# Performance work log

Hardware: AMD Instinct MI355X
Metric: run time of the kernel (lower is better)

Reference implementation:

```python
import jax, jax.numpy as jnp
import numpy as np

NUM_EMBEDDINGS = 1024
EMBEDDING_DIM = 512
SAMPLE_TOKENS = 4
CODE_DIM = EMBEDDING_DIM // SAMPLE_TOKENS  # 128
COMMITMENT_COST = 0.25


def setup_inputs() -> dict:
    key = jax.random.key(0)
    k1, k2 = jax.random.split(key)
    inputs = jax.random.normal(k1, (16, 1024, EMBEDDING_DIM), dtype=jnp.float32)
    # nn.Embedding weight init: uniform(-1/K, 1/K)
    emb_weight = jax.random.uniform(
        k2, (NUM_EMBEDDINGS, CODE_DIM), dtype=jnp.float32,
        minval=-1.0 / NUM_EMBEDDINGS, maxval=1.0 / NUM_EMBEDDINGS)
    return {"inputs": inputs, "emb_weight": emb_weight}


def reference(inputs, emb_weight):
    input_shape = inputs.shape
    flat = inputs.reshape(-1, CODE_DIM)  # [N, d]
    distances = (jnp.sum(flat * flat, axis=1, keepdims=True)
                 + jnp.sum(emb_weight * emb_weight, axis=1)
                 - 2.0 * jnp.matmul(flat, emb_weight.T))  # [N, K]
    encoding_indices = jnp.argmin(distances, axis=1)  # [N]
    # gather codebook rows instead of one-hot matmul (same math)
    quantized = jnp.take(emb_weight, encoding_indices, axis=0).reshape(input_shape)

    e_latent_loss = jnp.mean((jax.lax.stop_gradient(quantized) - inputs) ** 2)
    q_latent_loss = jnp.mean((quantized - jax.lax.stop_gradient(inputs)) ** 2)
    loss = q_latent_loss + COMMITMENT_COST * e_latent_loss

    # straight-through estimator
    quantized_ste = inputs + jax.lax.stop_gradient(quantized - inputs)

    # avg_probs = mean of one-hot encodings = code-usage histogram / N
    n = flat.shape[0]
    counts = jnp.zeros((NUM_EMBEDDINGS,), dtype=jnp.float32).at[encoding_indices].add(1.0)
    avg_probs = counts / n
    perplexity = jnp.exp(-jnp.sum(avg_probs * jnp.log(avg_probs + 1e-10)))

    return (quantized_ste, loss, perplexity)
```

## Files before the change

### kernel.cpp

```cpp
#include <hip/hip_runtime.h>
#include <cmath>

#define DIM      128
#define NELEMS   8388608
#define BAND_INT 12288

typedef __attribute__((ext_vector_type(8))) short  short8;
typedef __attribute__((ext_vector_type(4))) float  f32x4;


__device__ inline unsigned short f2bf(float x) {
    unsigned u = __float_as_uint(x);
    unsigned r = u + 0x7FFFu + ((u >> 16) & 1u);
    return (unsigned short)(r >> 16);
}

__global__ __launch_bounds__(256) void vq_prep_kernel(
        const float* __restrict__ e, unsigned short* __restrict__ Ehi,
        float* __restrict__ Bsq, int* __restrict__ counts, double* __restrict__ sse) {
    const int tid = threadIdx.x;
    {
        const int t  = blockIdx.x * 256 + tid;
        const int c  = t >> 4;
        const int gs = t & 15;
        const int kt = gs >> 2, qd = gs & 3;
        const int d0 = gs * 8;
        const float4 v0 = *(const float4*)(e + c * DIM + d0);
        const float4 v1 = *(const float4*)(e + c * DIM + d0 + 4);
        float f[8] = {v0.x, v0.y, v0.z, v0.w, v1.x, v1.y, v1.z, v1.w};
        unsigned short h[8];
        #pragma unroll
        for (int j = 0; j < 8; ++j) h[j] = f2bf(f[j]);
        const int ct = c >> 4, n = c & 15;
        uint4 ph;
        ph.x = h[0] | (h[1] << 16); ph.y = h[2] | (h[3] << 16);
        ph.z = h[4] | (h[5] << 16); ph.w = h[6] | (h[7] << 16);
        *(uint4*)&Ehi[(((ct * 4 + kt) * 64 + qd * 16 + n) * 8)] = ph;
    }
    {
        const int lane = tid & 31;
        #pragma unroll
        for (int r2 = 0; r2 < 2; ++r2) {
            const int row = blockIdx.x * 16 + (tid >> 5) * 2 + r2;
            const float4 xv = *(const float4*)(e + (size_t)row * DIM + lane * 4);
            float s = xv.x * xv.x + xv.y * xv.y + xv.z * xv.z + xv.w * xv.w;
            #pragma unroll
            for (int off = 16; off > 0; off >>= 1) s += __shfl_xor(s, off);
            if (lane == 0) Bsq[row] = s;
        }
    }
    if (blockIdx.x == 0) {
        ((int4*)counts)[tid] = make_int4(0, 0, 0, 0);
        if (tid == 0) *sse = 0.0;
    }
}

#define LOADPAIR(BUF, P)                                                        \
    do {                                                                        \
        const unsigned short* _bp = Ehi + (size_t)(P) * 4096;                   \
        _Pragma("unroll")                                                       \
        for (int _c = 0; _c < 2; ++_c)                                          \
            _Pragma("unroll")                                                   \
            for (int _kt = 0; _kt < 4; ++_kt)                                   \
                BUF[_c][_kt] = *(const short8*)&_bp[((_c * 4 + _kt) * 64 + lane) * 8]; \
    } while (0)

#define COMPUTEPAIR(BUF, P)                                                     \
    do {                                                                        \
        _Pragma("unroll")                                                       \
        for (int _c = 0; _c < 2; ++_c) {                                        \
            const int _ct = 2 * (P) + _c;                                       \
            f32x4 _a0 = cinit, _a1 = cinit;                                     \
            _Pragma("unroll")                                                   \
            for (int _kt = 0; _kt < 4; ++_kt) {                                 \
                _a0 = __builtin_amdgcn_mfma_f32_16x16x32_bf16(Af[0][_kt], BUF[_c][_kt], _a0, 0, 0, 0); \
                _a1 = __builtin_amdgcn_mfma_f32_16x16x32_bf16(Af[1][_kt], BUF[_c][_kt], _a1, 0, 0, 0); \
            }                                                                   \
            _Pragma("unroll")                                                   \
            for (int _r = 0; _r < 4; ++_r) {                                    \
                const int _k0 = (__float_as_int(_a0[_r]) & (int)0xFFFFFFC0) | _ct; \
                const int _t0 = min(K1[_r], _k0);                               \
                K1[_r] = max(K1[_r], _k0);                                      \
                K2[_r] = max(K2[_r], _t0);                                      \
                const int _k1 = (__float_as_int(_a1[_r]) & (int)0xFFFFFFC0) | _ct; \
                const int _t1 = min(K1[4 + _r], _k1);                           \
                K1[4 + _r] = max(K1[4 + _r], _k1);                              \
                K2[4 + _r] = max(K2[4 + _r], _t1);                              \
            }                                                                   \
        }                                                                       \
    } while (0)

__global__ __launch_bounds__(256) void vq_main_kernel(
        const float* __restrict__ x, const float* __restrict__ emb,
        const unsigned short* __restrict__ Ehi, const float* __restrict__ Bsq,
        int* __restrict__ counts, double* __restrict__ sse,
        float* __restrict__ out) {
    __shared__ unsigned short Xs[16384];
    __shared__ float sAsq[128];
    __shared__ int   sidx[128];
    __shared__ float pblk[2];

    const int tid  = threadIdx.x;
    const int wave = tid >> 6;
    const int lane = tid & 63;
    const int n    = lane & 15;
    const int quad = lane >> 4;
    const int row0 = blockIdx.x * 128;

    {
        const int rl = tid >> 3, tq = tid & 7;
        const int dbase = tq * 16;
        const int rg_lo = rl >> 4, m = rl & 15;
        for (int w = 0; w < 4; ++w) {
            const int r = 32 * w + rl;
            const float* xp = x + (size_t)(row0 + r) * DIM + dbase;
            float p[4];
            #pragma unroll
            for (int q = 0; q < 4; ++q) {
                const float4 v = *(const float4*)(xp + 4 * q);
                p[q] = v.x * v.x + v.y * v.y + v.z * v.z + v.w * v.w;
                const int dd = dbase + 4 * q;
                const int kt = dd >> 5, qd = (dd >> 3) & 3, j = dd & 7;
                unsigned short h0 = f2bf(v.x), h1 = f2bf(v.y), h2 = f2bf(v.z), h3 = f2bf(v.w);
                uint2 ph;
                ph.x = h0 | (h1 << 16); ph.y = h2 | (h3 << 16);
                const int rg = w * 2 + rg_lo;
                *(uint2*)&Xs[(((rg * 4 + kt) * 64 + qd * 16 + m) * 8) + j] = ph;
            }
            #pragma unroll
            for (int q = 0; q < 4; ++q) p[q] += __shfl_xor(p[q], 4);
            #pragma unroll
            for (int q = 0; q < 4; ++q) p[q] += __shfl_xor(p[q], 2);
            #pragma unroll
            for (int q = 0; q < 4; ++q) p[q] += __shfl_xor(p[q], 1);
            const float s = (p[0] + p[2]) + (p[1] + p[3]);
            if (tq == 0) sAsq[r] = s;
        }
    }
    __syncthreads();

    short8 Af[2][4];
    #pragma unroll
    for (int rti = 0; rti < 2; ++rti)
        #pragma unroll
        for (int kt = 0; kt < 4; ++kt)
            Af[rti][kt] = *(const short8*)&Xs[(((wave * 2 + rti) * 4 + kt) * 64 + lane) * 8];
    __syncthreads();

    int K1[8], K2[8];
    #pragma unroll
    for (int i = 0; i < 8; ++i) { K1[i] = (int)0x80000000; K2[i] = (int)0x80000000; }

    const f32x4 cinit = {1.0f, 1.0f, 1.0f, 1.0f};

    short8 BfA[2][4], BfB[2][4];
    LOADPAIR(BfA, 0);
    for (int u = 0; u < 16; ++u) {
        const int pA = 2 * u, pB = 2 * u + 1;
        LOADPAIR(BfB, pB);
        COMPUTEPAIR(BfA, pA);
        if (pA + 2 < 32) LOADPAIR(BfA, pA + 2);
        COMPUTEPAIR(BfB, pB);
    }

    int* sc = (int*)&Xs[0];
    #pragma unroll
    for (int r8 = 0; r8 < 8; ++r8) {
        const int lr = 32 * wave + 16 * (r8 >> 2) + quad * 4 + (r8 & 3);
        ((int2*)sc)[lr * 16 + n] = make_int2(K1[r8], K2[r8]);
    }
    __syncthreads();

    if (tid < 128) {
        const int row  = tid;
        const int rowg = row0 + row;
        const int2* ent = (const int2*)sc + row * 16;
        int mx = (int)0x80000000;
        #pragma unroll
        for (int e2 = 0; e2 < 16; ++e2) mx = max(mx, ent[e2].x);
        const int thr = mx - BAND_INT;
        int ck[8];
        int nc = 0;
        #pragma unroll
        for (int e2 = 0; e2 < 16; ++e2) {
            const int2 kk = ent[e2];
            if (kk.x >= thr && nc < 8) ck[nc++] = ((kk.x & 63) << 4) | e2;
            if (kk.y >= thr && nc < 8) ck[nc++] = ((kk.y & 63) << 4) | e2;
        }
        float bd = INFINITY;
        int   bk = 0x7fffffff;
        const float4* xr = (const float4*)(x + (size_t)rowg * DIM);
        const float   aq = sAsq[row];
        for (int c = 0; c < nc; ++c) {
            const int k = ck[c];
            const float4* er = (const float4*)(emb + (size_t)k * DIM);
            float acc = 0.0f;
            #pragma unroll 4
            for (int dd = 0; dd < 32; ++dd) {
                const float4 xv = xr[dd];
                const float4 ev = er[dd];
                acc += xv.x * ev.x;
                acc += xv.y * ev.y;
                acc += xv.z * ev.z;
                acc += xv.w * ev.w;
            }
            const float t    = aq + Bsq[k];
            const float dist = t - 2.0f * acc;
            if (dist < bd || (dist == bd && k < bk)) { bd = dist; bk = k; }
        }
        sidx[row] = bk;
        atomicAdd(&counts[bk], 1);
        float ss = bd;
        #pragma unroll
        for (int off = 32; off > 0; off >>= 1) ss += __shfl_down(ss, off);
        if (lane == 0) pblk[wave] = ss;
    }
    __syncthreads();
    if (tid == 0) atomicAdd(sse, (double)(pblk[0] + pblk[1]));

    #pragma unroll
    for (int i = tid; i < 4096; i += 256) {
        const int row = i >> 5, d4 = i & 31;
        const int k = sidx[row];
        const float4 xv = *((const float4*)(x + (size_t)(row0 + row) * DIM) + d4);
        const float4 qv = *((const float4*)emb + (size_t)k * 32 + d4);
        float4 ov;
        ov.x = xv.x + (qv.x - xv.x);
        ov.y = xv.y + (qv.y - xv.y);
        ov.z = xv.z + (qv.z - xv.z);
        ov.w = xv.w + (qv.w - xv.w);
        *((float4*)out + (size_t)(row0 + row) * 32 + d4) = ov;
    }
}

__global__ __launch_bounds__(1024) void vq_finalize_kernel(
        const int* __restrict__ counts, const double* __restrict__ sse,
        float* __restrict__ out_tail) {
    __shared__ double red[1024];
    const int t = threadIdx.x;
    const float p = (float)counts[t] * (1.0f / 65536.0f);
    red[t] = (double)p * log((double)p + 1e-10);
    __syncthreads();
    for (int s = 512; s > 0; s >>= 1) {
        if (t < s) red[t] += red[t + s];
        __syncthreads();
    }
    if (t == 0) {
        const float m = (float)(*sse * (1.0 / 8388608.0));
        out_tail[0] = m + 0.25f * m;
        out_tail[1] = (float)exp(-red[0]);
    }
}

extern "C" void kernel_launch(void* const* d_in, const int* in_sizes, int n_in,
                              void* d_out, int out_size, void* d_ws, size_t ws_size,
                              hipStream_t stream) {
    const float* x   = (const float*)d_in[0];
    const float* emb = (const float*)d_in[1];
    float* out = (float*)d_out;

    char*           ws     = (char*)d_ws;
    float*          Bsq    = (float*)(ws + 0);
    int*            counts = (int*)(ws + 4096);
    double*         sse    = (double*)(ws + 8192);
    unsigned short* Ehi    = (unsigned short*)(ws + 16384);

    vq_prep_kernel<<<64, 256, 0, stream>>>(emb, Ehi, Bsq, counts, sse);
    vq_main_kernel<<<512, 256, 0, stream>>>(x, emb, Ehi, Bsq, counts, sse, out);
    vq_finalize_kernel<<<1, 1024, 0, stream>>>(counts, sse, out + NELEMS);
}
```

Before: 144.0 us.

## Split codebook across waves with 32-row blocks and parallel candidate rescoring

Each block now handles 32 rows instead of 128, and the four waves split the 1024 codes among themselves instead of each wave scanning all codes for its own rows. Grid size grows from 512 to 2048 blocks and LDS use shrinks. The exact fp32 rescoring of candidates now spreads across 8 threads per row with a shuffle argmin, replacing a serial loop over up to 8 candidates on half the threads. The cost is that every block reloads the full bf16 codebook for fewer rows, so codebook traffic per row rises.

After: 203.2 us. 41.1% more time.

```diff
diff --git a/kernel.cpp b/kernel.cpp
--- a/kernel.cpp
+++ b/kernel.cpp
@@ -95,47 +95,43 @@
         const unsigned short* __restrict__ Ehi, const float* __restrict__ Bsq,
         int* __restrict__ counts, double* __restrict__ sse,
         float* __restrict__ out) {
-    __shared__ unsigned short Xs[16384];
-    __shared__ float sAsq[128];
-    __shared__ int   sidx[128];
-    __shared__ float pblk[2];
+    __shared__ __align__(16) unsigned short Xs[8320];
+    __shared__ float sAsq[32];
+    __shared__ int   sidx[32];
+    __shared__ float pblk[4];
 
     const int tid  = threadIdx.x;
     const int wave = tid >> 6;
     const int lane = tid & 63;
     const int n    = lane & 15;
     const int quad = lane >> 4;
-    const int row0 = blockIdx.x * 128;
+    const int row0 = blockIdx.x * 32;
 
     {
         const int rl = tid >> 3, tq = tid & 7;
         const int dbase = tq * 16;
-        const int rg_lo = rl >> 4, m = rl & 15;
-        for (int w = 0; w < 4; ++w) {
-            const int r = 32 * w + rl;
-            const float* xp = x + (size_t)(row0 + r) * DIM + dbase;
-            float p[4];
-            #pragma unroll
-            for (int q = 0; q < 4; ++q) {
-                const float4 v = *(const float4*)(xp + 4 * q);
-                p[q] = v.x * v.x + v.y * v.y + v.z * v.z + v.w * v.w;
-                const int dd = dbase + 4 * q;
-                const int kt = dd >> 5, qd = (dd >> 3) & 3, j = dd & 7;
-                unsigned short h0 = f2bf(v.x), h1 = f2bf(v.y), h2 = f2bf(v.z), h3 = f2bf(v.w);
-                uint2 ph;
-                ph.x = h0 | (h1 << 16); ph.y = h2 | (h3 << 16);
-                const int rg = w * 2 + rg_lo;
-                *(uint2*)&Xs[(((rg * 4 + kt) * 64 + qd * 16 + m) * 8) + j] = ph;
-            }
-            #pragma unroll
-            for (int q = 0; q < 4; ++q) p[q] += __shfl_xor(p[q], 4);
-            #pragma unroll
-            for (int q = 0; q < 4; ++q) p[q] += __shfl_xor(p[q], 2);
-            #pragma unroll
-            for (int q = 0; q < 4; ++q) p[q] += __shfl_xor(p[q], 1);
-            const float s = (p[0] + p[2]) + (p[1] + p[3]);
-            if (tq == 0) sAsq[r] = s;
+        const int rg = rl >> 4, m = rl & 15;
+        const float* xp = x + (size_t)(row0 + rl) * DIM + dbase;
+        float p[4];
+        #pragma unroll
+        for (int q = 0; q < 4; ++q) {
+            const float4 v = *(const float4*)(xp + 4 * q);
+            p[q] = v.x * v.x + v.y * v.y + v.z * v.z + v.w * v.w;
+            const int dd = dbase + 4 * q;
+            const int kt = dd >> 5, qd = (dd >> 3) & 3, j = dd & 7;
+            unsigned short h0 = f2bf(v.x), h1 = f2bf(v.y), h2 = f2bf(v.z), h3 = f2bf(v.w);
+            uint2 ph;
+            ph.x = h0 | (h1 << 16); ph.y = h2 | (h3 << 16);
+            *(uint2*)&Xs[(((rg * 4 + kt) * 64 + qd * 16 + m) * 8) + j] = ph;
         }
+        #pragma unroll
+        for (int q = 0; q < 4; ++q) p[q] += __shfl_xor(p[q], 4);
+        #pragma unroll
+        for (int q = 0; q < 4; ++q) p[q] += __shfl_xor(p[q], 2);
+        #pragma unroll
+        for (int q = 0; q < 4; ++q) p[q] += __shfl_xor(p[q], 1);
+        const float s = (p[0] + p[2]) + (p[1] + p[3]);
+        if (tq == 0) sAsq[rl] = s;
     }
     __syncthreads();
 
@@ -144,7 +140,7 @@
     for (int rti = 0; rti < 2; ++rti)
         #pragma unroll
         for (int kt = 0; kt < 4; ++kt)
-            Af[rti][kt] = *(const short8*)&Xs[(((wave * 2 + rti) * 4 + kt) * 64 + lane) * 8];
+            Af[rti][kt] = *(const short8*)&Xs[(((rti * 4 + kt) * 64 + lane) * 8)];
     __syncthreads();
 
     int K1[8], K2[8];
@@ -154,72 +150,85 @@
     const f32x4 cinit = {1.0f, 1.0f, 1.0f, 1.0f};
 
     short8 BfA[2][4], BfB[2][4];
-    LOADPAIR(BfA, 0);
-    for (int u = 0; u < 16; ++u) {
-        const int pA = 2 * u, pB = 2 * u + 1;
+    const int pbase = wave * 8;
+    LOADPAIR(BfA, pbase);
+    for (int u = 0; u < 4; ++u) {
+        const int pA = pbase + 2 * u, pB = pA + 1;
         LOADPAIR(BfB, pB);
         COMPUTEPAIR(BfA, pA);
-        if (pA + 2 < 32) LOADPAIR(BfA, pA + 2);
+        if (u < 3) LOADPAIR(BfA, pA + 2);
         COMPUTEPAIR(BfB, pB);
     }
 
-    int* sc = (int*)&Xs[0];
+    int2* sc = (int2*)Xs;
     #pragma unroll
     for (int r8 = 0; r8 < 8; ++r8) {
-        const int lr = 32 * wave + 16 * (r8 >> 2) + quad * 4 + (r8 & 3);
-        ((int2*)sc)[lr * 16 + n] = make_int2(K1[r8], K2[r8]);
-    }
-    __syncthreads();
-
-    if (tid < 128) {
-        const int row  = tid;
-        const int rowg = row0 + row;
-        const int2* ent = (const int2*)sc + row * 16;
-        int mx = (int)0x80000000;
-        #pragma unroll
-        for (int e2 = 0; e2 < 16; ++e2) mx = max(mx, ent[e2].x);
-        const int thr = mx - BAND_INT;
-        int ck[8];
-        int nc = 0;
-        #pragma unroll
-        for (int e2 = 0; e2 < 16; ++e2) {
-            const int2 kk = ent[e2];
-            if (kk.x >= thr && nc < 8) ck[nc++] = ((kk.x & 63) << 4) | e2;
-            if (kk.y >= thr && nc < 8) ck[nc++] = ((kk.y & 63) << 4) | e2;
+        const int lr = 16 * (r8 >> 2) + quad * 4 + (r8 & 3);
+        sc[lr * 65 + wave * 16 + n] = make_int2(K1[r8], K2[r8]);
+    }
+    __syncthreads();
+
+    const int vrow = tid >> 3;
+    const int vj   = tid & 7;
+    const int2* ent = sc + vrow * 65;
+
+    int mx = (int)0x80000000;
+    #pragma unroll
+    for (int e = 0; e < 8; ++e) {
+        const int2 kk = ent[vj * 8 + e];
+        mx = max(mx, max(kk.x, kk.y));
+    }
+    mx = max(mx, __shfl_xor(mx, 4));
+    mx = max(mx, __shfl_xor(mx, 2));
+    mx = max(mx, __shfl_xor(mx, 1));
+    const int thr = mx - BAND_INT;
+
+    int myk = -1, seen = 0;
+    #pragma unroll 8
+    for (int e = 0; e < 64; ++e) {
+        const int2 kk = ent[e];
+        if (kk.x >= thr) { if (seen == vj) myk = ((kk.x & 63) << 4) | (e & 15); ++seen; }
+        if (kk.y >= thr) { if (seen == vj) myk = ((kk.y & 63) << 4) | (e & 15); ++seen; }
+    }
+
+    float bd = INFINITY;
+    int   bk = 0x7fffffff;
+    if (myk >= 0) {
+        const float4* xr = (const float4*)(x + (size_t)(row0 + vrow) * DIM);
+        const float4* er = (const float4*)(emb + (size_t)myk * DIM);
+        float acc = 0.0f;
+        #pragma unroll 4
+        for (int dd = 0; dd < 32; ++dd) {
+            const float4 xv = xr[dd];
+            const float4 ev = er[dd];
+            acc += xv.x * ev.x;
+            acc += xv.y * ev.y;
+            acc += xv.z * ev.z;
+            acc += xv.w * ev.w;
         }
-        float bd = INFINITY;
-        int   bk = 0x7fffffff;
-        const float4* xr = (const float4*)(x + (size_t)rowg * DIM);
-        const float   aq = sAsq[row];
-        for (int c = 0; c < nc; ++c) {
-            const int k = ck[c];
-            const float4* er = (const float4*)(emb + (size_t)k * DIM);
-            float acc = 0.0f;
-            #pragma unroll 4
-            for (int dd = 0; dd < 32; ++dd) {
-                const float4 xv = xr[dd];
-                const float4 ev = er[dd];
-                acc += xv.x * ev.x;
-                acc += xv.y * ev.y;
-                acc += xv.z * ev.z;
-                acc += xv.w * ev.w;
-            }
-            const float t    = aq + Bsq[k];
-            const float dist = t - 2.0f * acc;
-            if (dist < bd || (dist == bd && k < bk)) { bd = dist; bk = k; }
-        }
-        sidx[row] = bk;
+        const float t = sAsq[vrow] + Bsq[myk];
+        bd = t - 2.0f * acc;
+        bk = myk;
+    }
+    #pragma unroll
+    for (int off = 4; off > 0; off >>= 1) {
+        const float obd = __shfl_xor(bd, off);
+        const int   obk = __shfl_xor(bk, off);
+        if (obd < bd || (obd == bd && obk < bk)) { bd = obd; bk = obk; }
+    }
+    if (vj == 0) {
+        sidx[vrow] = bk;
         atomicAdd(&counts[bk], 1);
-        float ss = bd;
-        #pragma unroll
-        for (int off = 32; off > 0; off >>= 1) ss += __shfl_down(ss, off);
-        if (lane == 0) pblk[wave] = ss;
-    }
-    __syncthreads();
-    if (tid == 0) atomicAdd(sse, (double)(pblk[0] + pblk[1]));
-
-    #pragma unroll
-    for (int i = tid; i < 4096; i += 256) {
+    }
+    float contrib = (vj == 0) ? bd : 0.0f;
+    #pragma unroll
+    for (int off = 32; off > 0; off >>= 1) contrib += __shfl_xor(contrib, off);
+    if (lane == 0) pblk[wave] = contrib;
+    __syncthreads();
+    if (tid == 0) atomicAdd(sse, (double)((pblk[0] + pblk[1]) + (pblk[2] + pblk[3])));
+
+    #pragma unroll
+    for (int i = tid; i < 1024; i += 256) {
         const int row = i >> 5, d4 = i & 31;
         const int k = sidx[row];
         const float4 xv = *((const float4*)(x + (size_t)(row0 + row) * DIM) + d4);
@@ -266,6 +275,6 @@
     unsigned short* Ehi    = (unsigned short*)(ws + 16384);
 
     vq_prep_kernel<<<64, 256, 0, stream>>>(emb, Ehi, Bsq, counts, sse);
-    vq_main_kernel<<<512, 256, 0, stream>>>(x, emb, Ehi, Bsq, counts, sse, out);
+    vq_main_kernel<<<2048, 256, 0, stream>>>(x, emb, Ehi, Bsq, counts, sse, out);
     vq_finalize_kernel<<<1, 1024, 0, stream>>>(counts, sse, out + NELEMS);
 }
```

## Halve rows per block and split codebook across wave pairs

Applied to the files above, without the earlier changes.

Each block now handles 64 rows instead of 128, launching 1024 blocks. The four waves split the work: two wave groups each cover 32 rows and half of the codebook pairs. Partial top-2 keys from both halves are merged in shared memory, padded to a stride of 33 to reduce bank conflicts. The goal is more blocks across the 256 CUs, with smaller LDS and a launch-bounds hint for higher occupancy, at the cost of fewer rows per wave in the refinement stage and more SSE atomics.

Result: slower. 200.3 us (+39.1%).

```diff
diff --git a/kernel.cpp b/kernel.cpp
--- a/kernel.cpp
+++ b/kernel.cpp
@@ -90,28 +90,28 @@
         }                                                                       \
     } while (0)
 
-__global__ __launch_bounds__(256) void vq_main_kernel(
+__global__ __launch_bounds__(256, 4) void vq_main_kernel(
         const float* __restrict__ x, const float* __restrict__ emb,
         const unsigned short* __restrict__ Ehi, const float* __restrict__ Bsq,
         int* __restrict__ counts, double* __restrict__ sse,
         float* __restrict__ out) {
-    __shared__ unsigned short Xs[16384];
-    __shared__ float sAsq[128];
-    __shared__ int   sidx[128];
-    __shared__ float pblk[2];
+    __shared__ __align__(16) unsigned short Xs[8448];
+    __shared__ float sAsq[64];
+    __shared__ int   sidx[64];
 
     const int tid  = threadIdx.x;
     const int wave = tid >> 6;
     const int lane = tid & 63;
     const int n    = lane & 15;
     const int quad = lane >> 4;
-    const int row0 = blockIdx.x * 128;
+    const int row0 = blockIdx.x * 64;
 
     {
         const int rl = tid >> 3, tq = tid & 7;
         const int dbase = tq * 16;
         const int rg_lo = rl >> 4, m = rl & 15;
-        for (int w = 0; w < 4; ++w) {
+        #pragma unroll
+        for (int w = 0; w < 2; ++w) {
             const int r = 32 * w + rl;
             const float* xp = x + (size_t)(row0 + r) * DIM + dbase;
             float p[4];
@@ -140,11 +140,14 @@
     __syncthreads();
 
     short8 Af[2][4];
-    #pragma unroll
-    for (int rti = 0; rti < 2; ++rti)
-        #pragma unroll
-        for (int kt = 0; kt < 4; ++kt)
-            Af[rti][kt] = *(const short8*)&Xs[(((wave * 2 + rti) * 4 + kt) * 64 + lane) * 8];
+    {
+        const int h = wave & 1;
+        #pragma unroll
+        for (int rti = 0; rti < 2; ++rti)
+            #pragma unroll
+            for (int kt = 0; kt < 4; ++kt)
+                Af[rti][kt] = *(const short8*)&Xs[((((h * 2 + rti) * 4 + kt) * 64 + lane) * 8)];
+    }
     __syncthreads();
 
     int K1[8], K2[8];
@@ -154,38 +157,40 @@
     const f32x4 cinit = {1.0f, 1.0f, 1.0f, 1.0f};
 
     short8 BfA[2][4], BfB[2][4];
-    LOADPAIR(BfA, 0);
-    for (int u = 0; u < 16; ++u) {
-        const int pA = 2 * u, pB = 2 * u + 1;
+    const int pbase = (wave >> 1) * 16;
+    LOADPAIR(BfA, pbase);
+    for (int u = 0; u < 8; ++u) {
+        const int pA = pbase + 2 * u, pB = pA + 1;
         LOADPAIR(BfB, pB);
         COMPUTEPAIR(BfA, pA);
-        if (pA + 2 < 32) LOADPAIR(BfA, pA + 2);
+        if (u < 7) LOADPAIR(BfA, pA + 2);
         COMPUTEPAIR(BfB, pB);
     }
 
-    int* sc = (int*)&Xs[0];
+    int2* sc = (int2*)Xs;
     #pragma unroll
     for (int r8 = 0; r8 < 8; ++r8) {
-        const int lr = 32 * wave + 16 * (r8 >> 2) + quad * 4 + (r8 & 3);
-        ((int2*)sc)[lr * 16 + n] = make_int2(K1[r8], K2[r8]);
-    }
-    __syncthreads();
-
-    if (tid < 128) {
+        const int lr = 32 * (wave & 1) + 16 * (r8 >> 2) + quad * 4 + (r8 & 3);
+        sc[lr * 33 + (wave >> 1) * 16 + n] = make_int2(K1[r8], K2[r8]);
+    }
+    __syncthreads();
+
+    if (tid < 64) {
         const int row  = tid;
         const int rowg = row0 + row;
-        const int2* ent = (const int2*)sc + row * 16;
+        const int2* ent = (const int2*)sc + row * 33;
         int mx = (int)0x80000000;
         #pragma unroll
-        for (int e2 = 0; e2 < 16; ++e2) mx = max(mx, ent[e2].x);
+        for (int e2 = 0; e2 < 32; ++e2) mx = max(mx, ent[e2].x);
         const int thr = mx - BAND_INT;
         int ck[8];
         int nc = 0;
         #pragma unroll
-        for (int e2 = 0; e2 < 16; ++e2) {
+        for (int e2 = 0; e2 < 32; ++e2) {
             const int2 kk = ent[e2];
-            if (kk.x >= thr && nc < 8) ck[nc++] = ((kk.x & 63) << 4) | e2;
-            if (kk.y >= thr && nc < 8) ck[nc++] = ((kk.y & 63) << 4) | e2;
+            const int ne = e2 & 15;
+            if (kk.x >= thr && nc < 8) ck[nc++] = ((kk.x & 63) << 4) | ne;
+            if (kk.y >= thr && nc < 8) ck[nc++] = ((kk.y & 63) << 4) | ne;
         }
         float bd = INFINITY;
         int   bk = 0x7fffffff;
@@ -213,13 +218,12 @@
         float ss = bd;
         #pragma unroll
         for (int off = 32; off > 0; off >>= 1) ss += __shfl_down(ss, off);
-        if (lane == 0) pblk[wave] = ss;
-    }
-    __syncthreads();
-    if (tid == 0) atomicAdd(sse, (double)(pblk[0] + pblk[1]));
+        if (tid == 0) atomicAdd(sse, (double)ss);
+    }
+    __syncthreads();
 
     #pragma unroll
-    for (int i = tid; i < 4096; i += 256) {
+    for (int i = tid; i < 2048; i += 256) {
         const int row = i >> 5, d4 = i & 31;
         const int k = sidx[row];
         const float4 xv = *((const float4*)(x + (size_t)(row0 + row) * DIM) + d4);
@@ -266,6 +270,6 @@
     unsigned short* Ehi    = (unsigned short*)(ws + 16384);
 
     vq_prep_kernel<<<64, 256, 0, stream>>>(emb, Ehi, Bsq, counts, sse);
-    vq_main_kernel<<<512, 256, 0, stream>>>(x, emb, Ehi, Bsq, counts, sse, out);
+    vq_main_kernel<<<1024, 256, 0, stream>>>(x, emb, Ehi, Bsq, counts, sse, out);
     vq_finalize_kernel<<<1, 1024, 0, stream>>>(counts, sse, out + NELEMS);
 }
```
